# Kernel optimization log

Hardware: AMD Instinct MI355X
Metric: run time of the kernel (lower is better)

Reference implementation:

```python
import jax, jax.numpy as jnp
import numpy as np

MASK_TOKEN_ID = 50264
EPS = 1e-8  # torch F.cosine_similarity eps


def setup_inputs() -> dict:
    B, S, H, L = 16, 2048, 1024, 128
    key = jax.random.key(0)
    k1, k2, k3, k4, k5, k6, k7 = jax.random.split(key, 7)
    input_ids = jax.random.randint(k1, (B, S), 0, 50000, dtype=jnp.int64)
    # exactly one <mask> token per row (module reshapes masked_select to (1, H))
    input_ids = input_ids.at[:, 5].set(MASK_TOKEN_ID)
    q_event_output = jax.random.normal(k2, (B, S, H), dtype=jnp.float32)
    sequence_output = jax.random.normal(k3, (B, S, H), dtype=jnp.float32)
    labels = jax.random.randint(k4, (B * L,), 0, 2, dtype=jnp.int32)
    # guarantee sum(labels_i) > 0 for every example (no skipped batches)
    labels = labels.reshape(B, L).at[:, 0].set(1).reshape(B * L)
    ev_rand = jax.random.randint(k5, (B * L,), 0, 2, dtype=jnp.int32)
    events = jnp.maximum(ev_rand, labels)  # denominator set is a superset
    offsets = jax.random.randint(k6, (L,), 0, S, dtype=jnp.int64)
    lengths = jnp.full((B,), L, dtype=jnp.int32)  # uniform segment lengths
    W = jax.random.normal(k7, (H, H), dtype=jnp.float32) * (1.0 / np.sqrt(H))
    b = jnp.zeros((H,), dtype=jnp.float32)
    return {"input_ids": input_ids, "q_event_output": q_event_output,
            "sequence_output": sequence_output, "events": events,
            "labels": labels, "offsets": offsets, "lengths": lengths,
            "W": W, "b": b}


def reference(input_ids, q_event_output, sequence_output, events, labels,
              offsets, lengths, W, b):
    B, S, H = sequence_output.shape
    L = offsets.shape[0]
    # dense projection (nn.Linear)
    seq_p = jnp.einsum('bsh,oh->bso', sequence_output, W) + b
    q_p = jnp.einsum('bsh,oh->bso', q_event_output, W) + b
    # anchor x: projected q_event_output at the (single) <mask> position
    mask_pos = jnp.argmax(input_ids == MASK_TOKEN_ID, axis=1)          # [B]
    x = jnp.take_along_axis(q_p, mask_pos[:, None, None], axis=1)[:, 0]  # [B,H]
    # candidate event embeddings: same offsets reused per batch (idx resets
    # to 0 in the original loop), gathered from projected sequence_output
    ys = seq_p[:, offsets, :]                                          # [B,L,H]
    # cosine similarity (stable, torch-style eps clamp)
    xn = jnp.linalg.norm(x, axis=-1)                                   # [B]
    yn = jnp.linalg.norm(ys, axis=-1)                                  # [B,L]
    cos = jnp.einsum('bh,blh->bl', x, ys) / jnp.maximum(xn[:, None] * yn, EPS)
    e = jnp.exp(cos)                                                   # temperature = 1.0
    lab = labels.reshape(B, L).astype(e.dtype)
    ev = events.reshape(B, L).astype(e.dtype)
    numerator = jnp.sum(e * lab, axis=-1)
    denominator = jnp.sum(e * ev, axis=-1)
    clr_loss = -jnp.log(numerator / denominator)                       # [B]
    return jnp.mean(clr_loss)
```

## Files before the change

### kernel.cpp

```cpp
#include <hip/hip_runtime.h>
#include <hip/hip_bf16.h>

#define MASK_ID 50264
#define Bn 16
#define Sn 2048
#define Hn 1024
#define Ln 128

typedef __attribute__((ext_vector_type(8))) short short8;
typedef __attribute__((ext_vector_type(4))) float f32x4;

__device__ __forceinline__ unsigned short f2bf(float f) {
    __hip_bfloat16 h = __float2bfloat16(f);
    return __builtin_bit_cast(unsigned short, h);
}

__global__ __launch_bounds__(256) void pack_k(
        const int* __restrict__ ids, const float* __restrict__ q,
        const float* __restrict__ seq, const int* __restrict__ offsets,
        const float* __restrict__ W,
        unsigned short* __restrict__ Apk, unsigned short* __restrict__ Wpk,
        unsigned short* __restrict__ Qpk) {
    const int blk = blockIdx.x, tid = threadIdx.x;
    if (blk < 192) {
        const float* src;
        unsigned short* dst;
        if (blk < 128) {
            int by = blk >> 3, rg = blk & 7;
            src = seq + ((size_t)by * Sn + (size_t)offsets[rg * 16 + (tid & 15)]) * Hn;
            dst = Apk + (size_t)blk * 16384;
        } else {
            int cg = blk - 128;
            src = W + (size_t)(cg * 16 + (tid & 15)) * Hn;
            dst = Wpk + (size_t)cg * 16384;
        }
        #pragma unroll
        for (int i = 0; i < 8; ++i) {
            int c = i * 256 + tid;
            int koff = (c >> 4) * 8;
            float4 v0 = *(const float4*)(src + koff);
            float4 v1 = *(const float4*)(src + koff + 4);
            short8 o;
            o[0] = (short)f2bf(v0.x); o[1] = (short)f2bf(v0.y);
            o[2] = (short)f2bf(v0.z); o[3] = (short)f2bf(v0.w);
            o[4] = (short)f2bf(v1.x); o[5] = (short)f2bf(v1.y);
            o[6] = (short)f2bf(v1.z); o[7] = (short)f2bf(v1.w);
            *(short8*)(dst + (size_t)c * 8) = o;
        }
    } else {
        __shared__ int t4[4];
        int b = blk - 192;
        int lm = Sn;
        const int* idrow = ids + b * Sn;
        for (int s = tid; s < Sn; s += 256)
            if (idrow[s] == MASK_ID) lm = min(lm, s);
        #pragma unroll
        for (int m = 32; m; m >>= 1) lm = min(lm, __shfl_xor(lm, m));
        if ((tid & 63) == 0) t4[tid >> 6] = lm;
        __syncthreads();
        int mp = min(min(t4[0], t4[1]), min(t4[2], t4[3]));
        if (mp == Sn) mp = 0;
        float4 v = ((const float4*)(q + ((size_t)b * Sn + mp) * Hn))[tid];
        ((ushort4*)(Qpk + b * Hn))[tid] =
            make_ushort4(f2bf(v.x), f2bf(v.y), f2bf(v.z), f2bf(v.w));
    }
}

__global__ __launch_bounds__(256, 2) void gemm10_k(
        const unsigned short* __restrict__ Apk, const unsigned short* __restrict__ Wpk,
        const unsigned short* __restrict__ Qpk, const float* __restrict__ bias,
        float* __restrict__ yn2p, float* __restrict__ dotp, float* __restrict__ xn2p) {
    __shared__ float xvs[64];
    __shared__ float xred[4];
    __shared__ float red[128][2];

    const int blk = blockIdx.x, tid = threadIdx.x;
    const int wv = tid >> 6, l = tid & 63;
    const int x = blk & 7, ib = blk >> 3;
    const int by = (x >> 1) * 4 + (ib >> 3);
    const int bx = (x & 1) * 8 + (ib & 7);
    const int rbase = by * 128, cbase = bx * 64;
    const int l15 = l & 15;

    const char* aP0 = (const char*)Apk + ((size_t)((by * 8 + wv * 2) * 32) << 10) + (l << 4);
    const char* aP1 = aP0 + (32 << 10);
    const char* bP  = (const char*)Wpk + ((size_t)(bx * 4 * 32) << 10) + (l << 4);
    const char* qP  = (const char*)Qpk + (by << 11) + ((l >> 4) << 4);

    f32x4 acc[2][4];
    #pragma unroll
    for (int i = 0; i < 2; ++i)
        #pragma unroll
        for (int j = 0; j < 4; ++j) acc[i][j] = (f32x4){0.f, 0.f, 0.f, 0.f};
    f32x4 xacc = {0.f, 0.f, 0.f, 0.f};

    #pragma unroll 2
    for (int ks = 0; ks < 32; ++ks) {
        short8 a0 = *(const short8*)(aP0 + ks * 1024);
        short8 a1 = *(const short8*)(aP1 + ks * 1024);
        short8 b0 = *(const short8*)(bP + ks * 1024);
        short8 b1 = *(const short8*)(bP + ks * 1024 + 32768);
        short8 b2 = *(const short8*)(bP + ks * 1024 + 65536);
        short8 b3 = *(const short8*)(bP + ks * 1024 + 98304);
        short8 aq = *(const short8*)(qP + ks * 64);
        acc[0][0] = __builtin_amdgcn_mfma_f32_16x16x32_bf16(a0, b0, acc[0][0], 0, 0, 0);
        acc[0][1] = __builtin_amdgcn_mfma_f32_16x16x32_bf16(a0, b1, acc[0][1], 0, 0, 0);
        acc[0][2] = __builtin_amdgcn_mfma_f32_16x16x32_bf16(a0, b2, acc[0][2], 0, 0, 0);
        acc[0][3] = __builtin_amdgcn_mfma_f32_16x16x32_bf16(a0, b3, acc[0][3], 0, 0, 0);
        acc[1][0] = __builtin_amdgcn_mfma_f32_16x16x32_bf16(a1, b0, acc[1][0], 0, 0, 0);
        acc[1][1] = __builtin_amdgcn_mfma_f32_16x16x32_bf16(a1, b1, acc[1][1], 0, 0, 0);
        acc[1][2] = __builtin_amdgcn_mfma_f32_16x16x32_bf16(a1, b2, acc[1][2], 0, 0, 0);
        acc[1][3] = __builtin_amdgcn_mfma_f32_16x16x32_bf16(a1, b3, acc[1][3], 0, 0, 0);
        short8 bw = (wv == 0) ? b0 : (wv == 1) ? b1 : (wv == 2) ? b2 : b3;
        xacc = __builtin_amdgcn_mfma_f32_16x16x32_bf16(aq, bw, xacc, 0, 0, 0);
    }

    float bvx = bias[cbase + wv * 16 + l15];
    float xv_own = xacc[0] + bvx;
    if (l < 16) xvs[wv * 16 + l] = xv_own;
    {
        float px = (l < 16) ? xv_own * xv_own : 0.f;
        #pragma unroll
        for (int m = 1; m < 16; m <<= 1) px += __shfl_xor(px, m);
        if (l == 0) xred[wv] = px;
    }
    __syncthreads();

    float xv[4], bv[4];
    #pragma unroll
    for (int nf = 0; nf < 4; ++nf) {
        xv[nf] = xvs[nf * 16 + l15];
        bv[nf] = bias[cbase + nf * 16 + l15];
    }
    #pragma unroll
    for (int i = 0; i < 2; ++i) {
        #pragma unroll
        for (int reg = 0; reg < 4; ++reg) {
            float y2v = 0.f, xyv = 0.f;
            #pragma unroll
            for (int nf = 0; nf < 4; ++nf) {
                float y = acc[i][nf][reg] + bv[nf];
                y2v += y * y;
                xyv += xv[nf] * y;
            }
            #pragma unroll
            for (int m = 1; m < 16; m <<= 1) {
                y2v += __shfl_xor(y2v, m);
                xyv += __shfl_xor(xyv, m);
            }
            if (l15 == 0) {
                int lrow = wv * 32 + i * 16 + (l >> 4) * 4 + reg;
                red[lrow][0] = y2v;
                red[lrow][1] = xyv;
            }
        }
    }
    __syncthreads();
    if (tid < 128) yn2p[(size_t)(rbase + tid) * 16 + bx] = red[tid][0];
    else           dotp[(size_t)(rbase + tid - 128) * 16 + bx] = red[tid - 128][1];
    if (tid == 0)  xn2p[by * 16 + bx] = xred[0] + xred[1] + xred[2] + xred[3];
}

__global__ __launch_bounds__(1024) void final10_k(
        const float* __restrict__ yn2p, const float* __restrict__ dotp,
        const float* __restrict__ xn2p,
        const int* __restrict__ labels, const int* __restrict__ events,
        float* __restrict__ out) {
    __shared__ float xns[16], wn[32], wd[32], ln16[16];
    const int tid = threadIdx.x;
    const int w = tid >> 6, l = tid & 63;

    if (tid < 16) {
        const f32x4* p = (const f32x4*)(xn2p + tid * 16);
        f32x4 s4 = p[0] + p[1] + p[2] + p[3];
        xns[tid] = sqrtf(s4[0] + s4[1] + s4[2] + s4[3]);
    }
    __syncthreads();

    #pragma unroll
    for (int h = 0; h < 2; ++h) {
        int row = h * 1024 + tid;
        const f32x4* py = (const f32x4*)(yn2p + (size_t)row * 16);
        const f32x4* pd = (const f32x4*)(dotp + (size_t)row * 16);
        f32x4 sy = py[0] + py[1] + py[2] + py[3];
        f32x4 sd = pd[0] + pd[1] + pd[2] + pd[3];
        float y2 = sy[0] + sy[1] + sy[2] + sy[3];
        float dt = sd[0] + sd[1] + sd[2] + sd[3];
        int b = row >> 7;
        float c = dt / fmaxf(xns[b] * sqrtf(y2), 1e-8f);
        float e = expf(c);
        float numt = e * (float)labels[row];
        float dent = e * (float)events[row];
        #pragma unroll
        for (int m = 32; m; m >>= 1) { numt += __shfl_xor(numt, m); dent += __shfl_xor(dent, m); }
        if (l == 0) { wn[h * 16 + w] = numt; wd[h * 16 + w] = dent; }
    }
    __syncthreads();
    if (tid < 16) {
        int s0 = (tid >> 3) * 16 + (tid & 7) * 2;
        float num = wn[s0] + wn[s0 + 1];
        float den = wd[s0] + wd[s0 + 1];
        ln16[tid] = logf(den) - logf(num);
    }
    __syncthreads();
    if (w == 0) {
        float v = (l < 16) ? ln16[l] : 0.f;
        #pragma unroll
        for (int m = 32; m; m >>= 1) v += __shfl_xor(v, m);
        if (l == 0) out[0] = v * (1.0f / Bn);
    }
}

extern "C" void kernel_launch(void* const* d_in, const int* in_sizes, int n_in,
                              void* d_out, int out_size, void* d_ws, size_t ws_size,
                              hipStream_t stream) {
    const int*   input_ids = (const int*)d_in[0];
    const float* q         = (const float*)d_in[1];
    const float* seq       = (const float*)d_in[2];
    const int*   events    = (const int*)d_in[3];
    const int*   labels    = (const int*)d_in[4];
    const int*   offsets   = (const int*)d_in[5];
    const float* W         = (const float*)d_in[7];
    const float* bias      = (const float*)d_in[8];
    float* out = (float*)d_out;

    char* ws = (char*)d_ws;
    unsigned short* Apk = (unsigned short*)(ws);
    unsigned short* Wpk = (unsigned short*)(ws + 4194304);
    unsigned short* Qpk = (unsigned short*)(ws + 6291456);
    float* yn2p = (float*)(ws + 6324224);
    float* dotp = (float*)(ws + 6455296);
    float* xn2p = (float*)(ws + 6586368);

    pack_k  <<<208, 256, 0, stream>>>(input_ids, q, seq, offsets, W, Apk, Wpk, Qpk);
    gemm10_k<<<256, 256, 0, stream>>>(Apk, Wpk, Qpk, bias, yn2p, dotp, xn2p);
    final10_k<<<1, 1024, 0, stream>>>(yn2p, dotp, xn2p, labels, events, out);
}
```

Before: 36.23 us.

## Fuse bf16 packing and mask search into the GEMM kernel with register double buffering

Removes the separate pack kernel. The GEMM now gathers fp32 rows of seq and W directly, converts them to bf16 in registers, and does the per-block mask-position search and the q-row conversion into shared memory itself. A two-stage register prefetch (fA/fB) overlaps the global loads with the MFMA work. This saves one kernel launch and the round trip through the packed workspace. In exchange, every block re-reads fp32 data, twice the bytes of bf16, and W is converted again by each of the 16 row blocks. Every block also scans input_ids and sees added register pressure.

```diff
diff --git a/kernel.cpp b/kernel.cpp
--- a/kernel.cpp
+++ b/kernel.cpp
@@ -14,62 +14,29 @@
     __hip_bfloat16 h = __float2bfloat16(f);
     return __builtin_bit_cast(unsigned short, h);
 }
-
-__global__ __launch_bounds__(256) void pack_k(
+__device__ __forceinline__ short8 cvt8(float4 lo, float4 hi) {
+    short8 r;
+    r[0] = (short)f2bf(lo.x); r[1] = (short)f2bf(lo.y);
+    r[2] = (short)f2bf(lo.z); r[3] = (short)f2bf(lo.w);
+    r[4] = (short)f2bf(hi.x); r[5] = (short)f2bf(hi.y);
+    r[6] = (short)f2bf(hi.z); r[7] = (short)f2bf(hi.w);
+    return r;
+}
+
+struct Frag {
+    float4 a0l, a0h, a1l, a1h;
+    float4 b0l, b0h, b1l, b1h, b2l, b2h, b3l, b3h;
+};
+
+__global__ __launch_bounds__(256, 2) void gemm11_k(
         const int* __restrict__ ids, const float* __restrict__ q,
         const float* __restrict__ seq, const int* __restrict__ offsets,
-        const float* __restrict__ W,
-        unsigned short* __restrict__ Apk, unsigned short* __restrict__ Wpk,
-        unsigned short* __restrict__ Qpk) {
-    const int blk = blockIdx.x, tid = threadIdx.x;
-    if (blk < 192) {
-        const float* src;
-        unsigned short* dst;
-        if (blk < 128) {
-            int by = blk >> 3, rg = blk & 7;
-            src = seq + ((size_t)by * Sn + (size_t)offsets[rg * 16 + (tid & 15)]) * Hn;
-            dst = Apk + (size_t)blk * 16384;
-        } else {
-            int cg = blk - 128;
-            src = W + (size_t)(cg * 16 + (tid & 15)) * Hn;
-            dst = Wpk + (size_t)cg * 16384;
-        }
-        #pragma unroll
-        for (int i = 0; i < 8; ++i) {
-            int c = i * 256 + tid;
-            int koff = (c >> 4) * 8;
-            float4 v0 = *(const float4*)(src + koff);
-            float4 v1 = *(const float4*)(src + koff + 4);
-            short8 o;
-            o[0] = (short)f2bf(v0.x); o[1] = (short)f2bf(v0.y);
-            o[2] = (short)f2bf(v0.z); o[3] = (short)f2bf(v0.w);
-            o[4] = (short)f2bf(v1.x); o[5] = (short)f2bf(v1.y);
-            o[6] = (short)f2bf(v1.z); o[7] = (short)f2bf(v1.w);
-            *(short8*)(dst + (size_t)c * 8) = o;
-        }
-    } else {
-        __shared__ int t4[4];
-        int b = blk - 192;
-        int lm = Sn;
-        const int* idrow = ids + b * Sn;
-        for (int s = tid; s < Sn; s += 256)
-            if (idrow[s] == MASK_ID) lm = min(lm, s);
-        #pragma unroll
-        for (int m = 32; m; m >>= 1) lm = min(lm, __shfl_xor(lm, m));
-        if ((tid & 63) == 0) t4[tid >> 6] = lm;
-        __syncthreads();
-        int mp = min(min(t4[0], t4[1]), min(t4[2], t4[3]));
-        if (mp == Sn) mp = 0;
-        float4 v = ((const float4*)(q + ((size_t)b * Sn + mp) * Hn))[tid];
-        ((ushort4*)(Qpk + b * Hn))[tid] =
-            make_ushort4(f2bf(v.x), f2bf(v.y), f2bf(v.z), f2bf(v.w));
-    }
-}
-
-__global__ __launch_bounds__(256, 2) void gemm10_k(
-        const unsigned short* __restrict__ Apk, const unsigned short* __restrict__ Wpk,
-        const unsigned short* __restrict__ Qpk, const float* __restrict__ bias,
-        float* __restrict__ yn2p, float* __restrict__ dotp, float* __restrict__ xn2p) {
+        const float* __restrict__ W, const float* __restrict__ bias,
+        float* __restrict__ yn2p, float* __restrict__ dotp, float* __restrict__ xn2p)
+{
+    __shared__ int   offs[128];
+    __shared__ int   t4[4];
+    __shared__ unsigned short qs[1024];
     __shared__ float xvs[64];
     __shared__ float xred[4];
     __shared__ float red[128][2];
@@ -80,12 +47,36 @@
     const int by = (x >> 1) * 4 + (ib >> 3);
     const int bx = (x & 1) * 8 + (ib & 7);
     const int rbase = by * 128, cbase = bx * 64;
-    const int l15 = l & 15;
-
-    const char* aP0 = (const char*)Apk + ((size_t)((by * 8 + wv * 2) * 32) << 10) + (l << 4);
-    const char* aP1 = aP0 + (32 << 10);
-    const char* bP  = (const char*)Wpk + ((size_t)(bx * 4 * 32) << 10) + (l << 4);
-    const char* qP  = (const char*)Qpk + (by << 11) + ((l >> 4) << 4);
+    const int l15 = l & 15, kgrp = l >> 4;
+
+    if (tid < 128) offs[tid] = offsets[tid];
+
+    int lm = Sn;
+    const int* idrow = ids + by * Sn;
+    for (int s = tid; s < Sn; s += 256)
+        if (idrow[s] == MASK_ID) lm = min(lm, s);
+    #pragma unroll
+    for (int m = 32; m; m >>= 1) lm = min(lm, __shfl_xor(lm, m));
+    if (l == 0) t4[wv] = lm;
+    __syncthreads();
+    int mp = min(min(t4[0], t4[1]), min(t4[2], t4[3]));
+    if (mp == Sn) mp = 0;
+
+    {
+        float4 v = ((const float4*)(q + ((size_t)by * Sn + mp) * Hn))[tid];
+        ((ushort4*)qs)[tid] = make_ushort4(f2bf(v.x), f2bf(v.y), f2bf(v.z), f2bf(v.w));
+    }
+
+    const int lrow0 = wv * 32 + l15;
+    const int lrow1 = lrow0 + 16;
+    const float* aR0 = seq + ((size_t)by * Sn + (size_t)offs[lrow0]) * Hn + kgrp * 8;
+    const float* aR1 = seq + ((size_t)by * Sn + (size_t)offs[lrow1]) * Hn + kgrp * 8;
+    const float* bR0 = W + (size_t)(cbase +  0 + l15) * Hn + kgrp * 8;
+    const float* bR1 = W + (size_t)(cbase + 16 + l15) * Hn + kgrp * 8;
+    const float* bR2 = W + (size_t)(cbase + 32 + l15) * Hn + kgrp * 8;
+    const float* bR3 = W + (size_t)(cbase + 48 + l15) * Hn + kgrp * 8;
+    const char* qsB = (const char*)qs;
+    __syncthreads();
 
     f32x4 acc[2][4];
     #pragma unroll
@@ -94,26 +85,45 @@
         for (int j = 0; j < 4; ++j) acc[i][j] = (f32x4){0.f, 0.f, 0.f, 0.f};
     f32x4 xacc = {0.f, 0.f, 0.f, 0.f};
 
-    #pragma unroll 2
-    for (int ks = 0; ks < 32; ++ks) {
-        short8 a0 = *(const short8*)(aP0 + ks * 1024);
-        short8 a1 = *(const short8*)(aP1 + ks * 1024);
-        short8 b0 = *(const short8*)(bP + ks * 1024);
-        short8 b1 = *(const short8*)(bP + ks * 1024 + 32768);
-        short8 b2 = *(const short8*)(bP + ks * 1024 + 65536);
-        short8 b3 = *(const short8*)(bP + ks * 1024 + 98304);
-        short8 aq = *(const short8*)(qP + ks * 64);
-        acc[0][0] = __builtin_amdgcn_mfma_f32_16x16x32_bf16(a0, b0, acc[0][0], 0, 0, 0);
-        acc[0][1] = __builtin_amdgcn_mfma_f32_16x16x32_bf16(a0, b1, acc[0][1], 0, 0, 0);
-        acc[0][2] = __builtin_amdgcn_mfma_f32_16x16x32_bf16(a0, b2, acc[0][2], 0, 0, 0);
-        acc[0][3] = __builtin_amdgcn_mfma_f32_16x16x32_bf16(a0, b3, acc[0][3], 0, 0, 0);
-        acc[1][0] = __builtin_amdgcn_mfma_f32_16x16x32_bf16(a1, b0, acc[1][0], 0, 0, 0);
-        acc[1][1] = __builtin_amdgcn_mfma_f32_16x16x32_bf16(a1, b1, acc[1][1], 0, 0, 0);
-        acc[1][2] = __builtin_amdgcn_mfma_f32_16x16x32_bf16(a1, b2, acc[1][2], 0, 0, 0);
-        acc[1][3] = __builtin_amdgcn_mfma_f32_16x16x32_bf16(a1, b3, acc[1][3], 0, 0, 0);
-        short8 bw = (wv == 0) ? b0 : (wv == 1) ? b1 : (wv == 2) ? b2 : b3;
-        xacc = __builtin_amdgcn_mfma_f32_16x16x32_bf16(aq, bw, xacc, 0, 0, 0);
-    }
+    #define LOADF(F, ks_) do { \
+        (F).a0l = *(const float4*)(aR0 + (ks_) * 32); (F).a0h = *(const float4*)(aR0 + (ks_) * 32 + 4); \
+        (F).a1l = *(const float4*)(aR1 + (ks_) * 32); (F).a1h = *(const float4*)(aR1 + (ks_) * 32 + 4); \
+        (F).b0l = *(const float4*)(bR0 + (ks_) * 32); (F).b0h = *(const float4*)(bR0 + (ks_) * 32 + 4); \
+        (F).b1l = *(const float4*)(bR1 + (ks_) * 32); (F).b1h = *(const float4*)(bR1 + (ks_) * 32 + 4); \
+        (F).b2l = *(const float4*)(bR2 + (ks_) * 32); (F).b2h = *(const float4*)(bR2 + (ks_) * 32 + 4); \
+        (F).b3l = *(const float4*)(bR3 + (ks_) * 32); (F).b3h = *(const float4*)(bR3 + (ks_) * 32 + 4); \
+    } while (0)
+
+    #define COMPUTE(F, ks_) do { \
+        short8 a0 = cvt8((F).a0l, (F).a0h); \
+        short8 a1 = cvt8((F).a1l, (F).a1h); \
+        short8 b0 = cvt8((F).b0l, (F).b0h); \
+        short8 b1 = cvt8((F).b1l, (F).b1h); \
+        short8 b2 = cvt8((F).b2l, (F).b2h); \
+        short8 b3 = cvt8((F).b3l, (F).b3h); \
+        short8 aq = *(const short8*)(qsB + (ks_) * 64 + kgrp * 16); \
+        acc[0][0] = __builtin_amdgcn_mfma_f32_16x16x32_bf16(a0, b0, acc[0][0], 0, 0, 0); \
+        acc[0][1] = __builtin_amdgcn_mfma_f32_16x16x32_bf16(a0, b1, acc[0][1], 0, 0, 0); \
+        acc[0][2] = __builtin_amdgcn_mfma_f32_16x16x32_bf16(a0, b2, acc[0][2], 0, 0, 0); \
+        acc[0][3] = __builtin_amdgcn_mfma_f32_16x16x32_bf16(a0, b3, acc[0][3], 0, 0, 0); \
+        acc[1][0] = __builtin_amdgcn_mfma_f32_16x16x32_bf16(a1, b0, acc[1][0], 0, 0, 0); \
+        acc[1][1] = __builtin_amdgcn_mfma_f32_16x16x32_bf16(a1, b1, acc[1][1], 0, 0, 0); \
+        acc[1][2] = __builtin_amdgcn_mfma_f32_16x16x32_bf16(a1, b2, acc[1][2], 0, 0, 0); \
+        acc[1][3] = __builtin_amdgcn_mfma_f32_16x16x32_bf16(a1, b3, acc[1][3], 0, 0, 0); \
+        short8 bw = (wv == 0) ? b0 : (wv == 1) ? b1 : (wv == 2) ? b2 : b3; \
+        xacc = __builtin_amdgcn_mfma_f32_16x16x32_bf16(aq, bw, xacc, 0, 0, 0); \
+    } while (0)
+
+    Frag fA, fB;
+    LOADF(fA, 0);
+    for (int ks = 0; ks < 32; ks += 2) {
+        LOADF(fB, ks + 1);
+        COMPUTE(fA, ks);
+        if (ks + 2 < 32) LOADF(fA, ks + 2);
+        COMPUTE(fB, ks + 1);
+    }
+    #undef LOADF
+    #undef COMPUTE
 
     float bvx = bias[cbase + wv * 16 + l15];
     float xv_own = xacc[0] + bvx;
@@ -161,11 +171,12 @@
     if (tid == 0)  xn2p[by * 16 + bx] = xred[0] + xred[1] + xred[2] + xred[3];
 }
 
-__global__ __launch_bounds__(1024) void final10_k(
+__global__ __launch_bounds__(1024) void final11_k(
         const float* __restrict__ yn2p, const float* __restrict__ dotp,
         const float* __restrict__ xn2p,
         const int* __restrict__ labels, const int* __restrict__ events,
-        float* __restrict__ out) {
+        float* __restrict__ out)
+{
     __shared__ float xns[16], wn[32], wd[32], ln16[16];
     const int tid = threadIdx.x;
     const int w = tid >> 6, l = tid & 63;
@@ -225,14 +236,11 @@
     float* out = (float*)d_out;
 
     char* ws = (char*)d_ws;
-    unsigned short* Apk = (unsigned short*)(ws);
-    unsigned short* Wpk = (unsigned short*)(ws + 4194304);
-    unsigned short* Qpk = (unsigned short*)(ws + 6291456);
-    float* yn2p = (float*)(ws + 6324224);
-    float* dotp = (float*)(ws + 6455296);
-    float* xn2p = (float*)(ws + 6586368);
-
-    pack_k  <<<208, 256, 0, stream>>>(input_ids, q, seq, offsets, W, Apk, Wpk, Qpk);
-    gemm10_k<<<256, 256, 0, stream>>>(Apk, Wpk, Qpk, bias, yn2p, dotp, xn2p);
-    final10_k<<<1, 1024, 0, stream>>>(yn2p, dotp, xn2p, labels, events, out);
-}
+    float* yn2p = (float*)(ws);
+    float* dotp = (float*)(ws + 131072);
+    float* xn2p = (float*)(ws + 262144);
+
+    gemm11_k<<<256, 256, 0, stream>>>(input_ids, q, seq, offsets, W, bias,
+                                      yn2p, dotp, xn2p);
+    final11_k<<<1, 1024, 0, stream>>>(yn2p, dotp, xn2p, labels, events, out);
+}
```

Result: slower. 59.64 us (+64.6%).
